# Performance work log

Measured on AMD Instinct MI355X. Metric: run time of the kernel, lower is better.

The kernel has to match this reference:

```python
import jax, jax.numpy as jnp
import numpy as np

# dims: S samples, J u-functions, D outputs, P input dims, N data points
S, J, D, P, N = 8, 4, 4, 3, 1024
BG, BU, MG, MU = 32, 32, 10, 32  # g-RFF, u-RFF, g-inducing, u-inducing


def setup_inputs() -> dict:
    key = jax.random.key(0)
    ks = jax.random.split(key, 16)
    ts = jax.random.normal(ks[0], (N, P), dtype=jnp.float32)
    alphas = jax.random.uniform(ks[1], (D, P), minval=0.5, maxval=1.5)   # filter window precisions
    pgs = jax.random.uniform(ks[2], (D, P), minval=0.5, maxval=1.5)      # g kernel precisions (ls2pr)
    zgs = jnp.tile(jnp.linspace(-1.0, 1.0, MG, dtype=jnp.float32)[:, None], (1, P))  # g inducing inputs
    thetag = 2.0 * jax.random.normal(ks[3], (D, P, BG))                  # g spectral freqs
    betag = jax.random.uniform(ks[4], (S, D, P, BG), minval=0.0, maxval=2 * np.pi)
    wg = jax.random.normal(ks[5], (S, D, P, BG)) / np.sqrt(BG)           # g RFF weights
    qg = 0.1 * jax.random.normal(ks[6], (S, D, P, MG))                   # g canonical weights (compute_q)
    pus = jax.random.uniform(ks[7], (P,), minval=0.5, maxval=1.5)        # u cross-kernel precisions
    zus = jax.random.normal(ks[8], (MU, P))                              # u inducing inputs
    thetau = 2.0 * jax.random.normal(ks[9], (S, J, P, BU))               # u spectral freqs
    betau = jax.random.uniform(ks[10], (S, J, BU), minval=0.0, maxval=2 * np.pi)
    wu = jax.random.normal(ks[11], (S, J, BU)) / np.sqrt(BU)
    qu = 0.1 * jax.random.normal(ks[12], (S, J, MU))                     # u canonical weights
    ampu = jnp.float32(1.0)
    log_amps = 0.1 * jax.random.normal(ks[13], (D, J))
    W = jax.random.normal(ks[14], (P, D)) / np.sqrt(P)
    return dict(ts=ts, alphas=alphas, pgs=pgs, zgs=zgs, thetag=thetag, betag=betag,
                wg=wg, qg=qg, pus=pus, zus=zus, thetau=thetau, betau=betau,
                wu=wu, qu=qu, ampu=ampu, log_amps=log_amps, W=W)


def reference(ts, alphas, pgs, zgs, thetag, betag, wg, qg, pus, zus,
              thetau, betau, wu, qu, ampu, log_amps, W):
    """NPGPLayer.forward: f_d(t) = sum_j amps[d,j] * I_dj(t) + ts @ W, where
    I_dj(t) = ampu * int_{R^P} [prod_p exp(-alpha_dp tau_p^2) g_dp(tau_p)] u_j(t - tau) dtau,
    with g, u sampled via random-Fourier + canonical (inducing) features; all 1-D
    Gaussian x cosine integrals are closed-form (this is the math of integrals.full_I)."""
    pi = jnp.pi
    amps = jnp.exp(log_amps)  # [D,J]

    # ---------- Part A: u RFF terms.  Fourier transform of windowed g at om ----------
    om = thetau  # [S,J,P,BU]
    aE = alphas[None, None, :, :, None, None]            # [1,1,D,P,1,1]
    th = thetag[None, None, :, :, None, :]               # [1,1,D,P,1,BG]
    omE = om[:, :, None, :, :, None]                     # [S,J,1,P,BU,1]
    e1 = jnp.exp(-(th - omE) ** 2 / (4 * aE))
    e2 = jnp.exp(-(th + omE) ** 2 / (4 * aE))
    cb = jnp.cos(betag)[:, None, :, :, None, :]
    sb = jnp.sin(betag)[:, None, :, :, None, :]
    wgE = wg[:, None, :, :, None, :]
    # int exp(-a tau^2) cos(th tau + b) e^{-i om tau} dtau
    Ghat_rff = jnp.sum(0.5 * jnp.sqrt(pi / aE) * wgE * ((e1 + e2) * cb + 1j * (e1 - e2) * sb), axis=-1)  # [S,J,D,P,BU]

    A = alphas + pgs                                     # [D,P]
    zT = zgs.T                                           # [P,MG]
    mu = pgs[:, :, None] * zT[None] / A[:, :, None]      # [D,P,MG]
    rg = alphas[:, :, None] * pgs[:, :, None] * zT[None] ** 2 / A[:, :, None]
    decay = jnp.exp(-om[:, :, None, :, :] ** 2 / (4 * A[None, None, :, :, None]))        # [S,J,D,P,BU]
    phase_mu = jnp.exp(-1j * om[:, :, None, :, :, None] * mu[None, None, :, :, None, :])  # [S,J,D,P,BU,MG]
    can_coef = jnp.sqrt(pi / A)[..., None] * jnp.exp(-rg)                                 # [D,P,MG]
    Ghat_can = jnp.sum(qg[:, None, :, :, None, :] * can_coef[None, None, :, :, None, :] * phase_mu, axis=-1) * decay
    Ghat = Ghat_rff + Ghat_can                           # [S,J,D,P,BU] complex

    phase_t = jnp.exp(1j * om[..., None] * ts.T[None, None, :, None, :])  # [S,J,P,BU,N]
    combined = Ghat[..., None] * phase_t[:, :, None]     # [S,J,D,P,BU,N]
    prodp = jnp.prod(combined, axis=3)                   # [S,J,D,BU,N]  (product over input dims)
    cu = wu * jnp.exp(1j * betau)                        # [S,J,BU]
    F_rff = jnp.real(jnp.einsum('sjb,sjdbn->sjdn', cu, prodp))

    # ---------- Part B: u canonical (inducing) terms -- Gaussian x Gaussian integrals ----------
    c = jnp.transpose(ts[:, None, :] - zus[None, :, :], (2, 0, 1))  # [P,N,MU]
    Bm = alphas + pus[None, :]                           # [D,P]
    mp = pus[None, :, None, None] * c[None] / Bm[:, :, None, None]                 # [D,P,N,MU]
    rp = alphas[:, :, None, None] * pus[None, :, None, None] * c[None] ** 2 / Bm[:, :, None, None]
    spec = jnp.sqrt(pi / Bm)[:, :, None] * jnp.exp(-thetag ** 2 / (4 * Bm[:, :, None]))  # [D,P,BG]
    arg = thetag[:, :, None, None, :] * mp[..., None]    # [D,P,N,MU,BG]
    cosx, sinx = jnp.cos(arg), jnp.sin(arg)
    coef1 = wg * jnp.cos(betag) * spec[None]             # [S,D,P,BG]
    coef2 = wg * jnp.sin(betag) * spec[None]
    term_rff = (jnp.einsum('dpnmb,sdpb->sdpnm', cosx, coef1)
                - jnp.einsum('dpnmb,sdpb->sdpnm', sinx, coef2)) * jnp.exp(-rp)[None]
    Cm = Bm + pgs                                        # [D,P]
    diff = mp[..., None] - zT[None, :, None, None, :]    # [D,P,N,MU,MG]
    r2 = Bm[:, :, None, None, None] * pgs[:, :, None, None, None] * diff ** 2 / Cm[:, :, None, None, None]
    val = jnp.sqrt(pi / Cm)[:, :, None, None, None] * jnp.exp(-rp[..., None] - r2)
    term_can = jnp.einsum('dpnmg,sdpg->sdpnm', val, qg)
    Gg = term_rff + term_can                             # [S,D,P,N,MU]
    prodg = jnp.prod(Gg, axis=2)                         # [S,D,N,MU]
    F_can = jnp.einsum('sjm,sdnm->sjdn', qu, prodg)

    F = ampu * (F_rff + F_can)                           # [S,J,D,N]
    layer = jnp.einsum('dj,sjdn->snd', amps, F)          # amps-weighted sum over u functions
    return layer + ts @ W                                # residual connection (is_final_layer=False)
```

## Files before the change

### kernel.cpp

```cpp
#include <hip/hip_runtime.h>
#include <math.h>

#define S_ 8
#define J_ 4
#define D_ 4
#define P_ 3
#define N_ 1024
#define BG_ 32
#define BU_ 32
#define MG_ 10
#define MU_ 32

static constexpr float PI_F = 3.14159265358979323846f;

#define COEF_OFF    0
#define CANPART_OFF 8192

#define NB_CAN  2048
#define NB_COEF 128

__global__ __launch_bounds__(128, 4) void fused_kernel(
    const float* __restrict__ ts,     const float* __restrict__ alphas,
    const float* __restrict__ pgs,    const float* __restrict__ zgs,
    const float* __restrict__ thetag, const float* __restrict__ betag,
    const float* __restrict__ wg,     const float* __restrict__ qg,
    const float* __restrict__ pus,    const float* __restrict__ zus,
    const float* __restrict__ thetau, const float* __restrict__ betau,
    const float* __restrict__ wu,     const float* __restrict__ qu,
    const float* __restrict__ ampu_p, const float* __restrict__ log_amps,
    float* __restrict__ ws)
{
    int bid = blockIdx.x;
    int t   = threadIdx.x;

    if (bid < NB_CAN) {
        __shared__ float sc1[P_][BG_][S_];
        __shared__ float sc2[P_][BG_][S_];
        __shared__ float sqg[P_][MG_][S_];
        __shared__ float stg[P_][BG_];
        __shared__ float szg[P_][MG_];
        __shared__ float szu[P_][MU_];
        __shared__ float sts[2][P_];
        __shared__ float squ[S_][MU_];
        __shared__ float skmp[P_], skrp[P_], sksc[P_], skbc[P_];

        int d  = bid >> 9;
        int n0 = (bid & 511) * 2;
        float ampu = ampu_p[0];

        for (int i = t; i < P_*BG_*S_; i += 128) {
            int p = i >> 8, b = (i >> 3) & 31, s = i & 7;
            float alpha = alphas[d*P_ + p];
            float Bm = alpha + pus[p];
            float th = thetag[(d*P_ + p)*BG_ + b];
            float spec = sqrtf(PI_F / Bm) * __expf(-th*th*0.25f/Bm);
            float be = betag[((s*D_ + d)*P_ + p)*BG_ + b];
            float w  = wg   [((s*D_ + d)*P_ + p)*BG_ + b];
            float sb, cb; __sincosf(be, &sb, &cb);
            sc1[p][b][s] = w * cb * spec;
            sc2[p][b][s] = w * sb * spec;
        }
        for (int i = t; i < P_*MG_*S_; i += 128) {
            int p = i / (MG_*S_), r = i % (MG_*S_), g = r >> 3, s = r & 7;
            ((float*)sqg)[i] = qg[((s*D_ + d)*P_ + p)*MG_ + g];
        }
        for (int i = t; i < S_*MU_; i += 128) {
            int s = i >> 5, m = i & 31;
            float acc = 0.f;
            #pragma unroll
            for (int j = 0; j < J_; ++j)
                acc += __expf(log_amps[d*J_ + j]) * qu[(s*J_ + j)*MU_ + m];
            squ[s][m] = ampu * acc;
        }
        if (t < P_*BG_) ((float*)stg)[t] = thetag[d*P_*BG_ + t];
        if (t < P_*MG_) { int p = t / MG_, g = t % MG_; szg[p][g] = zgs[g*P_ + p]; }
        if (t < P_*MU_) { int p = t >> 5, m = t & 31; szu[p][m] = zus[m*P_ + p]; }
        if (t >= 96 && t < 96 + 2*P_) { int i = t - 96; sts[i/3][i%3] = ts[n0*P_ + i]; }
        if (t >= 112 && t < 112 + P_) {
            int p = t - 112;
            float alpha = alphas[d*P_ + p], pg = pgs[d*P_ + p], pu = pus[p];
            float Bm = alpha + pu, invB = 1.f / Bm;
            skmp[p] = pu * invB;
            skrp[p] = alpha * pu * invB;
            float Cm = Bm + pg, invC = 1.f / Cm;
            sksc[p] = sqrtf(PI_F * invC);
            skbc[p] = Bm * pg * invC;
        }
        __syncthreads();

        int m = t & 31, q = (t >> 5) & 1, nl = t >> 6;

        float pr0=1.f,pr1=1.f,pr2=1.f,pr3=1.f,pr4=1.f,pr5=1.f,pr6=1.f,pr7=1.f;

        #pragma unroll 1
        for (int p = 0; p < P_; ++p) {
            float c  = sts[nl][p] - szu[p][m];
            float mp = skmp[p] * c;
            float E  = __expf(-skrp[p] * c * c);
            float a0=0.f,a1=0.f,a2=0.f,a3=0.f,a4=0.f,a5=0.f,a6=0.f,a7=0.f;
            int b0 = q * 16;
            #pragma unroll 4
            for (int bb = 0; bb < 16; ++bb) {
                int b = b0 + bb;
                float sx, cx; __sincosf(stg[p][b] * mp, &sx, &cx);
                const float4* c1v = (const float4*)&sc1[p][b][0];
                const float4* c2v = (const float4*)&sc2[p][b][0];
                float4 u0 = c1v[0], u1 = c1v[1];
                float4 v0 = c2v[0], v1 = c2v[1];
                a0 += u0.x*cx - v0.x*sx;  a1 += u0.y*cx - v0.y*sx;
                a2 += u0.z*cx - v0.z*sx;  a3 += u0.w*cx - v0.w*sx;
                a4 += u1.x*cx - v1.x*sx;  a5 += u1.y*cx - v1.y*sx;
                a6 += u1.z*cx - v1.z*sx;  a7 += u1.w*cx - v1.w*sx;
            }
            int g0 = q * 5;
            #pragma unroll 1
            for (int gg = 0; gg < 5; ++gg) {
                int g = g0 + gg;
                float diff = mp - szg[p][g];
                float v = sksc[p] * __expf(-skbc[p]*diff*diff);
                const float4* qv = (const float4*)&sqg[p][g][0];
                float4 q0 = qv[0], q1 = qv[1];
                a0 += q0.x*v; a1 += q0.y*v; a2 += q0.z*v; a3 += q0.w*v;
                a4 += q1.x*v; a5 += q1.y*v; a6 += q1.z*v; a7 += q1.w*v;
            }
            a0 += __shfl_xor(a0, 32, 64); a1 += __shfl_xor(a1, 32, 64);
            a2 += __shfl_xor(a2, 32, 64); a3 += __shfl_xor(a3, 32, 64);
            a4 += __shfl_xor(a4, 32, 64); a5 += __shfl_xor(a5, 32, 64);
            a6 += __shfl_xor(a6, 32, 64); a7 += __shfl_xor(a7, 32, 64);
            pr0 *= E*a0; pr1 *= E*a1; pr2 *= E*a2; pr3 *= E*a3;
            pr4 *= E*a4; pr5 *= E*a5; pr6 *= E*a6; pr7 *= E*a7;
        }

        int n = n0 + nl;
        float prod[S_] = {pr0,pr1,pr2,pr3,pr4,pr5,pr6,pr7};
        #pragma unroll
        for (int s = 0; s < S_; ++s) {
            float val = squ[s][m] * prod[s];
            #pragma unroll
            for (int off = 16; off; off >>= 1) val += __shfl_xor(val, off, 32);
            if ((t & 63) == 0)
                ws[CANPART_OFF + (s*N_ + n)*D_ + d] = val;
        }
    } else {
        int gtid = (bid - NB_CAN) * 128 + t;
        int q  = gtid & 3;
        int bu = (gtid >> 2) & 31;
        int d  = (gtid >> 7) & 3;
        int j  = (gtid >> 9) & 3;
        int s  = gtid >> 11;
        float ampu = ampu_p[0];
        float G3r = 1.f, G3i = 0.f;
        #pragma unroll 1
        for (int p = 0; p < P_; ++p) {
            float alpha = alphas[d*P_ + p], pg = pgs[d*P_ + p];
            float om    = thetau[((s*J_ + j)*P_ + p)*BU_ + bu];
            float inv4a = 0.25f / alpha;
            float pref  = 0.5f * sqrtf(PI_F / alpha);
            float gr = 0.f, gi = 0.f;
            int b0 = q * 8;
            #pragma unroll 2
            for (int bb = 0; bb < 8; ++bb) {
                int b = b0 + bb;
                float th = thetag[(d*P_ + p)*BG_ + b];
                float dm = th - om, dpl = th + om;
                float e1 = __expf(-dm*dm*inv4a);
                float e2 = __expf(-dpl*dpl*inv4a);
                float be = betag[((s*D_ + d)*P_ + p)*BG_ + b];
                float w  = wg   [((s*D_ + d)*P_ + p)*BG_ + b];
                float sb, cb; __sincosf(be, &sb, &cb);
                gr += pref * w * (e1 + e2) * cb;
                gi += pref * w * (e1 - e2) * sb;
            }
            float A = alpha + pg, invA = 1.f / A;
            float decay = __expf(-om*om*0.25f*invA);
            float cc    = sqrtf(PI_F * invA);
            float cr = 0.f, ci = 0.f;
            int g0 = q * 3, gn = (q < 3) ? 3 : 1;
            #pragma unroll 1
            for (int gg = 0; gg < gn; ++gg) {
                int g = g0 + gg;
                float z  = zgs[g*P_ + p];
                float mu = pg * z * invA;
                float rg = alpha * pg * z * z * invA;
                float cg = cc * __expf(-rg);
                float qv = qg[((s*D_ + d)*P_ + p)*MG_ + g];
                float sm, cm; __sincosf(om * mu, &sm, &cm);
                cr += qv * cg * cm;
                ci -= qv * cg * sm;
            }
            #pragma unroll
            for (int off = 1; off < 4; off <<= 1) {
                gr += __shfl_xor(gr, off, 4);
                gi += __shfl_xor(gi, off, 4);
                cr += __shfl_xor(cr, off, 4);
                ci += __shfl_xor(ci, off, 4);
            }
            float Gr = gr + decay * cr;
            float Gi = gi + decay * ci;
            float nr = G3r*Gr - G3i*Gi;
            float ni = G3r*Gi + G3i*Gr;
            G3r = nr; G3i = ni;
        }
        if (q == 0) {
            float bv = betau[(s*J_ + j)*BU_ + bu];
            float wv = wu   [(s*J_ + j)*BU_ + bu];
            float sbu, cbu; __sincosf(bv, &sbu, &cbu);
            float cuR = wv * cbu, cuI = wv * sbu;
            float amp = ampu * __expf(log_amps[d*J_ + j]);
            int base = (((s*J_ + j)*BU_ + bu)*D_ + d) * 2;
            ws[COEF_OFF + base    ] = amp * (cuR*G3r - cuI*G3i);
            ws[COEF_OFF + base + 1] = amp * (cuR*G3i + cuI*G3r);
        }
    }
}

__global__ __launch_bounds__(256) void final_kernel(
    const float* __restrict__ ts, const float* __restrict__ thetau,
    const float* __restrict__ W,  const float* __restrict__ ws,
    float* __restrict__ out)
{
    __shared__ float sth[J_][P_][BU_];
    __shared__ float scf[J_*BU_][8];
    __shared__ float sW[P_][D_];

    int bid = blockIdx.x;
    int s  = bid >> 6;
    int n0 = (bid & 63) * 16;
    int t  = threadIdx.x;

    for (int i = t; i < J_*P_*BU_; i += 256) ((float*)sth)[i] = thetau[s*J_*P_*BU_ + i];
    for (int i = t; i < J_*BU_*8; i += 256)  ((float*)scf)[i] = ws[COEF_OFF + s*J_*BU_*8 + i];
    if (t < P_*D_) ((float*)sW)[t] = W[t];
    __syncthreads();

    int k = t & 15, nl = t >> 4;
    int n = n0 + nl;
    float t0 = ts[n*P_], t1 = ts[n*P_ + 1], t2 = ts[n*P_ + 2];

    float r0=0.f, r1=0.f, r2=0.f, r3=0.f;
    #pragma unroll 2
    for (int i = 0; i < 8; ++i) {
        int pair = i*16 + k;
        int j = i >> 1;
        int bu = (i & 1) * 16 + k;
        float phi = sth[j][0][bu]*t0 + sth[j][1][bu]*t1 + sth[j][2][bu]*t2;
        float sp, cp; __sincosf(phi, &sp, &cp);
        const float4* cfv = (const float4*)&scf[pair][0];
        float4 u = cfv[0], v = cfv[1];
        r0 += u.x*cp - u.y*sp;
        r1 += u.z*cp - u.w*sp;
        r2 += v.x*cp - v.y*sp;
        r3 += v.z*cp - v.w*sp;
    }
    #pragma unroll
    for (int off = 8; off; off >>= 1) {
        r0 += __shfl_xor(r0, off, 16);
        r1 += __shfl_xor(r1, off, 16);
        r2 += __shfl_xor(r2, off, 16);
        r3 += __shfl_xor(r3, off, 16);
    }
    if (k == 0) {
        const float* cpart = ws + CANPART_OFF + (s*N_ + n)*D_;
        float* o = out + (s*N_ + n)*D_;
        o[0] = cpart[0] + r0 + t0*sW[0][0] + t1*sW[1][0] + t2*sW[2][0];
        o[1] = cpart[1] + r1 + t0*sW[0][1] + t1*sW[1][1] + t2*sW[2][1];
        o[2] = cpart[2] + r2 + t0*sW[0][2] + t1*sW[1][2] + t2*sW[2][2];
        o[3] = cpart[3] + r3 + t0*sW[0][3] + t1*sW[1][3] + t2*sW[2][3];
    }
}

extern "C" void kernel_launch(void* const* d_in, const int* in_sizes, int n_in,
                              void* d_out, int out_size, void* d_ws, size_t ws_size,
                              hipStream_t stream)
{
    const float* ts       = (const float*)d_in[0];
    const float* alphas   = (const float*)d_in[1];
    const float* pgs      = (const float*)d_in[2];
    const float* zgs      = (const float*)d_in[3];
    const float* thetag   = (const float*)d_in[4];
    const float* betag    = (const float*)d_in[5];
    const float* wg       = (const float*)d_in[6];
    const float* qg       = (const float*)d_in[7];
    const float* pus      = (const float*)d_in[8];
    const float* zus      = (const float*)d_in[9];
    const float* thetau   = (const float*)d_in[10];
    const float* betau    = (const float*)d_in[11];
    const float* wu       = (const float*)d_in[12];
    const float* qu       = (const float*)d_in[13];
    const float* ampu     = (const float*)d_in[14];
    const float* log_amps = (const float*)d_in[15];
    const float* W        = (const float*)d_in[16];
    float* ws  = (float*)d_ws;
    float* out = (float*)d_out;

    fused_kernel<<<NB_CAN + NB_COEF, 128, 0, stream>>>(
        ts, alphas, pgs, zgs, thetag, betag, wg, qg,
        pus, zus, thetau, betau, wu, qu, ampu, log_amps, ws);
    final_kernel<<<512, 256, 0, stream>>>(ts, thetau, W, ws, out);
}
```

Measured before the change: 28.67 us.

## Double block size in fused kernel and re-split final kernel work per thread

The fused kernel now runs 256-thread blocks that each handle four data points instead of two. This spreads the per-block shared-memory setup of coefficients and inducing values over twice as many points. The final kernel now gives each point a 32-lane group that loops over J, instead of a 16-lane group looping over 8 pairs, and launches twice as many blocks with 8 points each. It also uses float4 loads and stores for the partial sums and outputs. Larger blocks may lower occupancy or leave fewer blocks to schedule, and the wider reductions add shuffle steps.

```diff
diff --git a/kernel.cpp b/kernel.cpp
--- a/kernel.cpp
+++ b/kernel.cpp
@@ -16,10 +16,10 @@
 #define COEF_OFF    0
 #define CANPART_OFF 8192
 
-#define NB_CAN  2048
-#define NB_COEF 128
-
-__global__ __launch_bounds__(128, 4) void fused_kernel(
+#define NB_CAN  1024
+#define NB_COEF 64
+
+__global__ __launch_bounds__(256, 4) void fused_kernel(
     const float* __restrict__ ts,     const float* __restrict__ alphas,
     const float* __restrict__ pgs,    const float* __restrict__ zgs,
     const float* __restrict__ thetag, const float* __restrict__ betag,
@@ -32,6 +32,7 @@
 {
     int bid = blockIdx.x;
     int t   = threadIdx.x;
+    float ampu = ampu_p[0];
 
     if (bid < NB_CAN) {
         __shared__ float sc1[P_][BG_][S_];
@@ -40,15 +41,14 @@
         __shared__ float stg[P_][BG_];
         __shared__ float szg[P_][MG_];
         __shared__ float szu[P_][MU_];
-        __shared__ float sts[2][P_];
+        __shared__ float sts[4][P_];
         __shared__ float squ[S_][MU_];
         __shared__ float skmp[P_], skrp[P_], sksc[P_], skbc[P_];
 
-        int d  = bid >> 9;
-        int n0 = (bid & 511) * 2;
-        float ampu = ampu_p[0];
-
-        for (int i = t; i < P_*BG_*S_; i += 128) {
+        int d  = bid >> 8;
+        int n0 = (bid & 255) * 4;
+
+        for (int i = t; i < P_*BG_*S_; i += 256) {
             int p = i >> 8, b = (i >> 3) & 31, s = i & 7;
             float alpha = alphas[d*P_ + p];
             float Bm = alpha + pus[p];
@@ -60,12 +60,12 @@
             sc1[p][b][s] = w * cb * spec;
             sc2[p][b][s] = w * sb * spec;
         }
-        for (int i = t; i < P_*MG_*S_; i += 128) {
+        for (int i = t; i < P_*MG_*S_; i += 256) {
             int p = i / (MG_*S_), r = i % (MG_*S_), g = r >> 3, s = r & 7;
             ((float*)sqg)[i] = qg[((s*D_ + d)*P_ + p)*MG_ + g];
         }
-        for (int i = t; i < S_*MU_; i += 128) {
-            int s = i >> 5, m = i & 31;
+        {
+            int s = t >> 5, m = t & 31;
             float acc = 0.f;
             #pragma unroll
             for (int j = 0; j < J_; ++j)
@@ -74,8 +74,11 @@
         }
         if (t < P_*BG_) ((float*)stg)[t] = thetag[d*P_*BG_ + t];
         if (t < P_*MG_) { int p = t / MG_, g = t % MG_; szg[p][g] = zgs[g*P_ + p]; }
-        if (t < P_*MU_) { int p = t >> 5, m = t & 31; szu[p][m] = zus[m*P_ + p]; }
-        if (t >= 96 && t < 96 + 2*P_) { int i = t - 96; sts[i/3][i%3] = ts[n0*P_ + i]; }
+        if (t >= 128 && t < 128 + P_*MU_) {
+            int i = t - 128; int p = i >> 5, m = i & 31;
+            szu[p][m] = zus[m*P_ + p];
+        }
+        if (t >= 96 && t < 96 + 4*P_) { int i = t - 96; sts[i/3][i%3] = ts[n0*P_ + i]; }
         if (t >= 112 && t < 112 + P_) {
             int p = t - 112;
             float alpha = alphas[d*P_ + p], pg = pgs[d*P_ + p], pu = pus[p];
@@ -133,22 +136,22 @@
 
         int n = n0 + nl;
         float prod[S_] = {pr0,pr1,pr2,pr3,pr4,pr5,pr6,pr7};
+        int s0 = q * 4;
         #pragma unroll
-        for (int s = 0; s < S_; ++s) {
+        for (int ss = 0; ss < 4; ++ss) {
+            int s = s0 + ss;
             float val = squ[s][m] * prod[s];
             #pragma unroll
             for (int off = 16; off; off >>= 1) val += __shfl_xor(val, off, 32);
-            if ((t & 63) == 0)
-                ws[CANPART_OFF + (s*N_ + n)*D_ + d] = val;
+            if (m == 0) ws[CANPART_OFF + (s*N_ + n)*D_ + d] = val;
         }
     } else {
-        int gtid = (bid - NB_CAN) * 128 + t;
+        int gtid = (bid - NB_CAN) * 256 + t;
         int q  = gtid & 3;
         int bu = (gtid >> 2) & 31;
         int d  = (gtid >> 7) & 3;
         int j  = (gtid >> 9) & 3;
         int s  = gtid >> 11;
-        float ampu = ampu_p[0];
         float G3r = 1.f, G3i = 0.f;
         #pragma unroll 1
         for (int p = 0; p < P_; ++p) {
@@ -214,7 +217,7 @@
     }
 }
 
-__global__ __launch_bounds__(256) void final_kernel(
+__global__ __launch_bounds__(256, 4) void final_kernel(
     const float* __restrict__ ts, const float* __restrict__ thetau,
     const float* __restrict__ W,  const float* __restrict__ ws,
     float* __restrict__ out)
@@ -224,8 +227,8 @@
     __shared__ float sW[P_][D_];
 
     int bid = blockIdx.x;
-    int s  = bid >> 6;
-    int n0 = (bid & 63) * 16;
+    int s  = bid >> 7;
+    int n0 = (bid & 127) * 8;
     int t  = threadIdx.x;
 
     for (int i = t; i < J_*P_*BU_; i += 256) ((float*)sth)[i] = thetau[s*J_*P_*BU_ + i];
@@ -233,19 +236,16 @@
     if (t < P_*D_) ((float*)sW)[t] = W[t];
     __syncthreads();
 
-    int k = t & 15, nl = t >> 4;
+    int k = t & 31, nl = t >> 5;
     int n = n0 + nl;
     float t0 = ts[n*P_], t1 = ts[n*P_ + 1], t2 = ts[n*P_ + 2];
 
     float r0=0.f, r1=0.f, r2=0.f, r3=0.f;
     #pragma unroll 2
-    for (int i = 0; i < 8; ++i) {
-        int pair = i*16 + k;
-        int j = i >> 1;
-        int bu = (i & 1) * 16 + k;
-        float phi = sth[j][0][bu]*t0 + sth[j][1][bu]*t1 + sth[j][2][bu]*t2;
+    for (int j = 0; j < J_; ++j) {
+        float phi = sth[j][0][k]*t0 + sth[j][1][k]*t1 + sth[j][2][k]*t2;
         float sp, cp; __sincosf(phi, &sp, &cp);
-        const float4* cfv = (const float4*)&scf[pair][0];
+        const float4* cfv = (const float4*)&scf[j*BU_ + k][0];
         float4 u = cfv[0], v = cfv[1];
         r0 += u.x*cp - u.y*sp;
         r1 += u.z*cp - u.w*sp;
@@ -253,19 +253,20 @@
         r3 += v.z*cp - v.w*sp;
     }
     #pragma unroll
-    for (int off = 8; off; off >>= 1) {
-        r0 += __shfl_xor(r0, off, 16);
-        r1 += __shfl_xor(r1, off, 16);
-        r2 += __shfl_xor(r2, off, 16);
-        r3 += __shfl_xor(r3, off, 16);
+    for (int off = 16; off; off >>= 1) {
+        r0 += __shfl_xor(r0, off, 32);
+        r1 += __shfl_xor(r1, off, 32);
+        r2 += __shfl_xor(r2, off, 32);
+        r3 += __shfl_xor(r3, off, 32);
     }
     if (k == 0) {
-        const float* cpart = ws + CANPART_OFF + (s*N_ + n)*D_;
-        float* o = out + (s*N_ + n)*D_;
-        o[0] = cpart[0] + r0 + t0*sW[0][0] + t1*sW[1][0] + t2*sW[2][0];
-        o[1] = cpart[1] + r1 + t0*sW[0][1] + t1*sW[1][1] + t2*sW[2][1];
-        o[2] = cpart[2] + r2 + t0*sW[0][2] + t1*sW[1][2] + t2*sW[2][2];
-        o[3] = cpart[3] + r3 + t0*sW[0][3] + t1*sW[1][3] + t2*sW[2][3];
+        const float4 cpart = *(const float4*)(ws + CANPART_OFF + (s*N_ + n)*D_);
+        float4 o;
+        o.x = cpart.x + r0 + t0*sW[0][0] + t1*sW[1][0] + t2*sW[2][0];
+        o.y = cpart.y + r1 + t0*sW[0][1] + t1*sW[1][1] + t2*sW[2][1];
+        o.z = cpart.z + r2 + t0*sW[0][2] + t1*sW[1][2] + t2*sW[2][2];
+        o.w = cpart.w + r3 + t0*sW[0][3] + t1*sW[1][3] + t2*sW[2][3];
+        *(float4*)(out + (s*N_ + n)*D_) = o;
     }
 }
 
@@ -293,8 +294,8 @@
     float* ws  = (float*)d_ws;
     float* out = (float*)d_out;
 
-    fused_kernel<<<NB_CAN + NB_COEF, 128, 0, stream>>>(
+    fused_kernel<<<NB_CAN + NB_COEF, 256, 0, stream>>>(
         ts, alphas, pgs, zgs, thetag, betag, wg, qg,
         pus, zus, thetau, betau, wu, qu, ampu, log_amps, ws);
-    final_kernel<<<512, 256, 0, stream>>>(ts, thetau, W, ws, out);
+    final_kernel<<<1024, 256, 0, stream>>>(ts, thetau, W, ws, out);
 }
```

Result: faster. 27.08 us (-5.5%).
